# Kernel optimization log

Hardware: AMD Instinct MI355X
Metric: run time of the kernel (lower is better)

Reference implementation:

```python
import jax, jax.numpy as jnp
import numpy as np

B, N, D, KD = 8, 2048, 64, 64

def setup_inputs() -> dict:
    key = jax.random.key(0)
    ks = jax.random.split(key, 7)
    s = 1.0 / np.sqrt(D)
    return {
        "x":  jax.random.normal(ks[0], (B, N, D), dtype=jnp.float32),
        "Wq": jax.random.normal(ks[1], (D, KD), dtype=jnp.float32) * s,
        "bq": jnp.zeros((KD,), jnp.float32),
        "Wk": jax.random.normal(ks[2], (D, KD), dtype=jnp.float32) * s,
        "bk": jnp.zeros((KD,), jnp.float32),
        "Wv": jax.random.normal(ks[3], (D, KD), dtype=jnp.float32) * s,
        "bv": jnp.zeros((KD,), jnp.float32),
    }

def reference(x, Wq, bq, Wk, bk, Wv, bv):
    # Q,K,V: [B,N,KD]
    Q = x @ Wq + bq
    K = x @ Wk + bk
    V = x @ Wv + bv
    # scores: [B,N,N] (note: original applies NO 1/sqrt(d) scaling)
    scores = jnp.einsum('bij,bkj->bik', Q, K)
    probs = jax.nn.softmax(scores, axis=-1)
    # mean-threshold sparsification: keep entries above the row mean
    mask = (probs > jnp.mean(probs, axis=-1, keepdims=True)).astype(probs.dtype)
    sparse = probs * mask
    out = jnp.einsum('bij,bjk->bik', sparse, V)  # [B,N,KD]
    return out
```

## Files before the change

kernel.cpp:

```cpp
#include <hip/hip_runtime.h>

#define NB 8
#define NS 2048
#define ND 64
#define LOG2E 1.44269504f
#define QSC 256.0f
#define IQS (1.0f / 256.0f)

typedef _Float16 half8 __attribute__((ext_vector_type(8)));
typedef short short8 __attribute__((ext_vector_type(8)));
typedef __attribute__((ext_vector_type(4))) float floatx4;

__device__ __forceinline__ half8 cvt8(const float* p) {
    float4 a = *(const float4*)p;
    float4 b = *(const float4*)(p + 4);
    half8 h = {(_Float16)a.x, (_Float16)a.y, (_Float16)a.z, (_Float16)a.w,
               (_Float16)b.x, (_Float16)b.y, (_Float16)b.z, (_Float16)b.w};
    return h;
}
__device__ __forceinline__ half8 cvtWcol(const float* base) {
    half8 h;
#pragma unroll
    for (int j = 0; j < 8; ++j) h[j] = (_Float16)base[j * 64];
    return h;
}

__global__ __launch_bounds__(256) void qkv_proj(
    const float* __restrict__ x,
    const float* __restrict__ Wq, const float* __restrict__ bq,
    const float* __restrict__ Wk, const float* __restrict__ bk,
    const float* __restrict__ Wv, const float* __restrict__ bv,
    _Float16* __restrict__ Qg, _Float16* __restrict__ Kg,
    _Float16* __restrict__ Vt)
{
    __shared__ _Float16 vt[64 * 18];

    const int tid  = threadIdx.x;
    const int wv   = tid >> 6;
    const int l    = tid & 63;
    const int quad = l >> 4;
    const int tx   = l & 15;

    const int b  = blockIdx.x & 7;
    const int n0 = (blockIdx.x >> 3) * 16;

    const float* xr = x + ((size_t)b * NS + n0 + tx) * ND + quad * 8;
    half8 a0 = cvt8(xr);
    half8 a1 = cvt8(xr + 32);

    const floatx4 zf = {0.f, 0.f, 0.f, 0.f};

#pragma unroll
    for (int i = 0; i < 3; ++i) {
        const int ct = wv * 3 + i;
        const int m  = ct >> 2;
        const int lcol = (ct & 3) * 16 + tx;

        const float* Wm;
        const float* Bm;
        if (m == 0)      { Wm = Wq; Bm = bq; }
        else if (m == 1) { Wm = Wk; Bm = bk; }
        else             { Wm = Wv; Bm = bv; }

        half8 b0 = cvtWcol(Wm + (quad * 8) * 64 + lcol);
        half8 b1 = cvtWcol(Wm + (32 + quad * 8) * 64 + lcol);

        floatx4 acc = __builtin_amdgcn_mfma_f32_16x16x32_f16(a0, b0, zf, 0, 0, 0);
        acc = __builtin_amdgcn_mfma_f32_16x16x32_f16(a1, b1, acc, 0, 0, 0);
        const float bias = Bm[lcol];

        if (m == 0) {
#pragma unroll
            for (int r = 0; r < 4; ++r)
                Qg[((size_t)b * NS + n0 + quad * 4 + r) * ND + lcol] =
                    (_Float16)((acc[r] + bias) * LOG2E);
        } else if (m == 1) {
#pragma unroll
            for (int r = 0; r < 4; ++r)
                Kg[((size_t)b * NS + n0 + quad * 4 + r) * ND + lcol] = (_Float16)(acc[r] + bias);
        } else {
#pragma unroll
            for (int r = 0; r < 4; ++r)
                vt[lcol * 18 + quad * 4 + r] = (_Float16)(acc[r] + bias);
        }
    }
    __syncthreads();
    {
        const int d = tid >> 2, seg = tid & 3;
        uint2 p = *(uint2*)&vt[d * 18 + seg * 4];
        *(uint2*)(Vt + ((size_t)b * ND + d) * NS + n0 + seg * 4) = p;
    }
}

__global__ __launch_bounds__(512, 2) void attn(
    const _Float16* __restrict__ Qg,
    const _Float16* __restrict__ Kg,
    const _Float16* __restrict__ Vt,
    short* __restrict__ ct,
    float* __restrict__ out)
{
    __shared__ __align__(16) _Float16 smem[2 * 64 * 136];
    __shared__ float lsh[4 * 64];

    const int tid  = threadIdx.x;
    const int wv   = tid >> 6;
    const int l    = tid & 63;
    const int quad = l >> 4;
    const int tx   = l & 15;
    const int h    = wv >> 2;
    const int kq   = wv & 3;

    const int b  = blockIdx.x & 7;
    const int q0 = (blockIdx.x >> 3) * 64;

    const _Float16* Qb = Qg + ((size_t)b * NS + q0 + h * 32) * ND;
    const _Float16* Kb = Kg + (size_t)b * NS * ND;
    const _Float16* Vb = Vt + (size_t)b * ND * NS;
    short* ctb = ct + ((size_t)b * NS + q0) * NS;

    half8 qf[2][2];
#pragma unroll
    for (int rh = 0; rh < 2; ++rh)
#pragma unroll
        for (int kc = 0; kc < 2; ++kc)
            qf[rh][kc] = *(const half8*)(Qb + (size_t)(rh * 16 + tx) * ND + kc * 32 + quad * 8);

    const floatx4 zf = {0.f, 0.f, 0.f, 0.f};

    {
        const int skey = tid >> 3;
        const int sc   = (tid & 7) * 8;
        const _Float16* Ksrc = Kb + (size_t)skey * ND + sc;
        const int sdst = skey * 72 + sc;
        const int krow = (kq * 16 + tx) * 72;

        short* cst0 = ctb + (size_t)(h * 32 + tx) * NS + kq * 16 + quad * 4;
        short* cst1 = cst0 + (size_t)16 * NS;

        float lacc0 = 0.f, lacc1 = 0.f;

        uint4 gk = *(const uint4*)Ksrc;
        *(uint4*)(smem + sdst) = gk;
        for (int t = 0; t < 32; ++t) {
            const int buf = (t & 1) * 4608;
            __syncthreads();
            if (t < 31) gk = *(const uint4*)(Ksrc + (size_t)(t + 1) * 64 * ND);
            half8 kf0 = *(const half8*)(smem + buf + krow + quad * 8);
            half8 kf1 = *(const half8*)(smem + buf + krow + 32 + quad * 8);
#pragma unroll
            for (int rh = 0; rh < 2; ++rh) {
                floatx4 c = __builtin_amdgcn_mfma_f32_16x16x32_f16(kf0, qf[rh][0], zf, 0, 0, 0);
                c = __builtin_amdgcn_mfma_f32_16x16x32_f16(kf1, qf[rh][1], c, 0, 0, 0);
                int ci[4];
                float ladd = 0.f;
#pragma unroll
                for (int r = 0; r < 4; ++r) {
                    float cs = fminf(fmaxf(c[r] * QSC, -32767.f), 32767.f);
                    int ic = (int)rintf(cs);
                    ci[r] = ic;
                    ladd += __builtin_amdgcn_exp2f((float)ic * IQS);
                }
                if (rh == 0) lacc0 += ladd; else lacc1 += ladd;
                uint2 pk;
                pk.x = (unsigned)(ci[0] & 0xffff) | ((unsigned)(ci[1] & 0xffff) << 16);
                pk.y = (unsigned)(ci[2] & 0xffff) | ((unsigned)(ci[3] & 0xffff) << 16);
                *(uint2*)((rh ? cst1 : cst0) + (size_t)t * 64) = pk;
            }
            if (t < 31) *(uint4*)(smem + (buf ^ 4608) + sdst) = gk;
        }

#pragma unroll
        for (int off = 16; off < 64; off <<= 1) {
            lacc0 += __shfl_xor(lacc0, off);
            lacc1 += __shfl_xor(lacc1, off);
        }
        if (quad == 0) {
            lsh[kq * 64 + h * 32 + tx]      = lacc0;
            lsh[kq * 64 + h * 32 + 16 + tx] = lacc1;
        }
    }

    const int sdim = tid >> 4;
    const int sseg = (tid & 15) * 8;
    const _Float16* Vsrc0 = Vb + (size_t)sdim * NS + sseg;
    const _Float16* Vsrc1 = Vb + (size_t)(sdim + 32) * NS + sseg;
    const int vdst0 = sdim * 136 + sseg;
    const int vdst1 = (sdim + 32) * 136 + sseg;

    const short* crd0 = ctb + (size_t)(h * 32 + tx) * NS + kq * 32 + quad * 8;
    const short* crd1 = crd0 + (size_t)16 * NS;

    uint4 gv0 = *(const uint4*)Vsrc0;
    uint4 gv1 = *(const uint4*)Vsrc1;
    short8 ca0 = *(const short8*)crd0;
    short8 ca1 = *(const short8*)crd1;

    __syncthreads();

    float lg2L0, lg2L1;
    {
        const int row = h * 32 + tx;
        float L0 = lsh[row] + lsh[64 + row] + lsh[128 + row] + lsh[192 + row];
        float L1 = lsh[row + 16] + lsh[64 + row + 16] + lsh[128 + row + 16] + lsh[192 + row + 16];
        lg2L0 = __builtin_amdgcn_logf(L0);
        lg2L1 = __builtin_amdgcn_logf(L1);
    }

    *(uint4*)(smem + vdst0) = gv0;
    *(uint4*)(smem + vdst1) = gv1;

    floatx4 o[2][4] = {{zf, zf, zf, zf}, {zf, zf, zf, zf}};

    for (int t = 0; t < 16; ++t) {
        const int buf = (t & 1) * 8704;
        __syncthreads();
        short8 cn0, cn1;
        if (t < 15) {
            gv0 = *(const uint4*)(Vsrc0 + (size_t)(t + 1) * 128);
            gv1 = *(const uint4*)(Vsrc1 + (size_t)(t + 1) * 128);
            cn0 = *(const short8*)(crd0 + (size_t)(t + 1) * 128);
            cn1 = *(const short8*)(crd1 + (size_t)(t + 1) * 128);
        }
        half8 a0, a1;
#pragma unroll
        for (int j = 0; j < 8; ++j) {
            float d0 = (float)ca0[j] * IQS - lg2L0;
            a0[j] = (d0 > -11.f) ? (_Float16)__builtin_amdgcn_exp2f(d0) : (_Float16)0.f;
            float d1 = (float)ca1[j] * IQS - lg2L1;
            a1[j] = (d1 > -11.f) ? (_Float16)__builtin_amdgcn_exp2f(d1) : (_Float16)0.f;
        }
#pragma unroll
        for (int dg = 0; dg < 4; ++dg) {
            half8 vf = *(const half8*)(smem + buf + (dg * 16 + tx) * 136 + kq * 32 + quad * 8);
            o[0][dg] = __builtin_amdgcn_mfma_f32_16x16x32_f16(a0, vf, o[0][dg], 0, 0, 0);
            o[1][dg] = __builtin_amdgcn_mfma_f32_16x16x32_f16(a1, vf, o[1][dg], 0, 0, 0);
        }
        if (t < 15) {
            *(uint4*)(smem + (buf ^ 8704) + vdst0) = gv0;
            *(uint4*)(smem + (buf ^ 8704) + vdst1) = gv1;
            ca0 = cn0; ca1 = cn1;
        }
    }

    __syncthreads();
    float* osm = (float*)smem;
    if (kq == 0) {
#pragma unroll
        for (int rt = 0; rt < 2; ++rt)
#pragma unroll
            for (int dg = 0; dg < 4; ++dg)
#pragma unroll
                for (int r = 0; r < 4; ++r)
                    osm[(h * 32 + rt * 16 + quad * 4 + r) * 68 + dg * 16 + tx] = o[rt][dg][r];
    }
    __syncthreads();
    if (kq == 1) {
#pragma unroll
        for (int rt = 0; rt < 2; ++rt)
#pragma unroll
            for (int dg = 0; dg < 4; ++dg)
#pragma unroll
                for (int r = 0; r < 4; ++r)
                    osm[(h * 32 + rt * 16 + quad * 4 + r) * 68 + dg * 16 + tx] += o[rt][dg][r];
    }
    __syncthreads();
    if (kq == 2) {
#pragma unroll
        for (int rt = 0; rt < 2; ++rt)
#pragma unroll
            for (int dg = 0; dg < 4; ++dg)
#pragma unroll
                for (int r = 0; r < 4; ++r)
                    osm[(h * 32 + rt * 16 + quad * 4 + r) * 68 + dg * 16 + tx] += o[rt][dg][r];
    }
    __syncthreads();
    if (kq == 3) {
#pragma unroll
        for (int rt = 0; rt < 2; ++rt)
#pragma unroll
            for (int dg = 0; dg < 4; ++dg)
#pragma unroll
                for (int r = 0; r < 4; ++r)
                    out[((size_t)b * NS + q0 + h * 32 + rt * 16 + quad * 4 + r) * ND + dg * 16 + tx] =
                        osm[(h * 32 + rt * 16 + quad * 4 + r) * 68 + dg * 16 + tx] + o[rt][dg][r];
    }
}

extern "C" void kernel_launch(void* const* d_in, const int* in_sizes, int n_in,
                              void* d_out, int out_size, void* d_ws, size_t ws_size,
                              hipStream_t stream) {
    const float* x  = (const float*)d_in[0];
    const float* Wq = (const float*)d_in[1];
    const float* bq = (const float*)d_in[2];
    const float* Wk = (const float*)d_in[3];
    const float* bk = (const float*)d_in[4];
    const float* Wv = (const float*)d_in[5];
    const float* bv = (const float*)d_in[6];

    _Float16* Qg = (_Float16*)d_ws;
    _Float16* Kg = Qg + (size_t)NB * NS * ND;
    _Float16* Vt = Kg + (size_t)NB * NS * ND;
    short*    ct = (short*)(Vt + (size_t)NB * NS * ND);

    qkv_proj<<<NB * (NS / 16), 256, 0, stream>>>(x, Wq, bq, Wk, bk, Wv, bv, Qg, Kg, Vt);
    attn<<<NB * (NS / 64), 512, 0, stream>>>(Qg, Kg, Vt, ct, (float*)d_out);
}
```

Measured before the change: 122.8 us.

## Recompute QK^T scores in second pass instead of storing quantized scores

The attention kernel no longer writes int16-quantized scores to a global scratch buffer and rereads them. The second pass recomputes QK^T from K tiles in shared memory, applies exp2 with a mean threshold (L/N) and normalises by 1/L, then multiplies by V. This removes a large global write/read of B*N*N shorts at the cost of doubling the score MFMA work. A separate wprep kernel pre-transposes the weights to fp16, and qkv_proj now handles 64 rows per block to cut weight reloads.

```diff
diff --git a/kernel.cpp b/kernel.cpp
--- a/kernel.cpp
+++ b/kernel.cpp
@@ -4,11 +4,9 @@
 #define NS 2048
 #define ND 64
 #define LOG2E 1.44269504f
-#define QSC 256.0f
-#define IQS (1.0f / 256.0f)
 
 typedef _Float16 half8 __attribute__((ext_vector_type(8)));
-typedef short short8 __attribute__((ext_vector_type(8)));
+typedef _Float16 half4 __attribute__((ext_vector_type(4)));
 typedef __attribute__((ext_vector_type(4))) float floatx4;
 
 __device__ __forceinline__ half8 cvt8(const float* p) {
@@ -18,22 +16,27 @@
                (_Float16)b.x, (_Float16)b.y, (_Float16)b.z, (_Float16)b.w};
     return h;
 }
-__device__ __forceinline__ half8 cvtWcol(const float* base) {
-    half8 h;
-#pragma unroll
-    for (int j = 0; j < 8; ++j) h[j] = (_Float16)base[j * 64];
-    return h;
+
+__global__ __launch_bounds__(256) void wprep(
+    const float* __restrict__ Wq, const float* __restrict__ Wk,
+    const float* __restrict__ Wv, _Float16* __restrict__ Wt)
+{
+    const int m = blockIdx.x;
+    const float* W = (m == 0) ? Wq : (m == 1) ? Wk : Wv;
+    for (int i = threadIdx.x; i < 64 * 64; i += 256) {
+        const int c = i >> 6, d = i & 63;
+        Wt[((size_t)m * 64 + c) * 64 + d] = (_Float16)W[d * 64 + c];
+    }
 }
 
 __global__ __launch_bounds__(256) void qkv_proj(
-    const float* __restrict__ x,
-    const float* __restrict__ Wq, const float* __restrict__ bq,
-    const float* __restrict__ Wk, const float* __restrict__ bk,
-    const float* __restrict__ Wv, const float* __restrict__ bv,
+    const float* __restrict__ x, const _Float16* __restrict__ Wt,
+    const float* __restrict__ bq, const float* __restrict__ bk,
+    const float* __restrict__ bv,
     _Float16* __restrict__ Qg, _Float16* __restrict__ Kg,
     _Float16* __restrict__ Vt)
 {
-    __shared__ _Float16 vt[64 * 18];
+    __shared__ _Float16 vt[4][64 * 20];
 
     const int tid  = threadIdx.x;
     const int wv   = tid >> 6;
@@ -42,7 +45,7 @@
     const int tx   = l & 15;
 
     const int b  = blockIdx.x & 7;
-    const int n0 = (blockIdx.x >> 3) * 16;
+    const int n0 = (blockIdx.x >> 3) * 64 + wv * 16;
 
     const float* xr = x + ((size_t)b * NS + n0 + tx) * ND + quad * 8;
     half8 a0 = cvt8(xr);
@@ -51,23 +54,19 @@
     const floatx4 zf = {0.f, 0.f, 0.f, 0.f};
 
 #pragma unroll
-    for (int i = 0; i < 3; ++i) {
-        const int ct = wv * 3 + i;
-        const int m  = ct >> 2;
-        const int lcol = (ct & 3) * 16 + tx;
-
-        const float* Wm;
-        const float* Bm;
-        if (m == 0)      { Wm = Wq; Bm = bq; }
-        else if (m == 1) { Wm = Wk; Bm = bk; }
-        else             { Wm = Wv; Bm = bv; }
-
-        half8 b0 = cvtWcol(Wm + (quad * 8) * 64 + lcol);
-        half8 b1 = cvtWcol(Wm + (32 + quad * 8) * 64 + lcol);
+    for (int ctile = 0; ctile < 12; ++ctile) {
+        const int m    = ctile >> 2;
+        const int lcol = (ctile & 3) * 16 + tx;
+
+        const _Float16* Wb = Wt + ((size_t)m * 64 + lcol) * 64;
+        half8 b0 = *(const half8*)(Wb + quad * 8);
+        half8 b1 = *(const half8*)(Wb + 32 + quad * 8);
 
         floatx4 acc = __builtin_amdgcn_mfma_f32_16x16x32_f16(a0, b0, zf, 0, 0, 0);
         acc = __builtin_amdgcn_mfma_f32_16x16x32_f16(a1, b1, acc, 0, 0, 0);
-        const float bias = Bm[lcol];
+
+        const float* Bp = (m == 0) ? bq : (m == 1) ? bk : bv;
+        const float bias = Bp[lcol];
 
         if (m == 0) {
 #pragma unroll
@@ -77,18 +76,27 @@
         } else if (m == 1) {
 #pragma unroll
             for (int r = 0; r < 4; ++r)
-                Kg[((size_t)b * NS + n0 + quad * 4 + r) * ND + lcol] = (_Float16)(acc[r] + bias);
+                Kg[((size_t)b * NS + n0 + quad * 4 + r) * ND + lcol] =
+                    (_Float16)(acc[r] + bias);
         } else {
 #pragma unroll
             for (int r = 0; r < 4; ++r)
-                vt[lcol * 18 + quad * 4 + r] = (_Float16)(acc[r] + bias);
+                vt[wv][lcol * 20 + quad * 4 + r] = (_Float16)(acc[r] + bias);
         }
     }
     __syncthreads();
     {
-        const int d = tid >> 2, seg = tid & 3;
-        uint2 p = *(uint2*)&vt[d * 18 + seg * 4];
-        *(uint2*)(Vt + ((size_t)b * ND + d) * NS + n0 + seg * 4) = p;
+        const int d = l;
+        const _Float16* src = &vt[wv][d * 20];
+        uint2 p0 = *(const uint2*)(src);
+        uint2 p1 = *(const uint2*)(src + 4);
+        uint2 p2 = *(const uint2*)(src + 8);
+        uint2 p3 = *(const uint2*)(src + 12);
+        uint4 q0 = {p0.x, p0.y, p1.x, p1.y};
+        uint4 q1 = {p2.x, p2.y, p3.x, p3.y};
+        _Float16* dst = Vt + ((size_t)b * ND + d) * NS + n0;
+        *(uint4*)(dst)     = q0;
+        *(uint4*)(dst + 8) = q1;
     }
 }
 
@@ -96,11 +104,13 @@
     const _Float16* __restrict__ Qg,
     const _Float16* __restrict__ Kg,
     const _Float16* __restrict__ Vt,
-    short* __restrict__ ct,
     float* __restrict__ out)
 {
-    __shared__ __align__(16) _Float16 smem[2 * 64 * 136];
+    __shared__ __align__(16) _Float16 smem[2 * 64 * 72 + 2 * 64 * 72];
     __shared__ float lsh[4 * 64];
+
+    _Float16* ksm = smem;
+    _Float16* vsm = smem + 2 * 64 * 72;
 
     const int tid  = threadIdx.x;
     const int wv   = tid >> 6;
@@ -116,7 +126,6 @@
     const _Float16* Qb = Qg + ((size_t)b * NS + q0 + h * 32) * ND;
     const _Float16* Kb = Kg + (size_t)b * NS * ND;
     const _Float16* Vb = Vt + (size_t)b * ND * NS;
-    short* ctb = ct + ((size_t)b * NS + q0) * NS;
 
     half8 qf[2][2];
 #pragma unroll
@@ -125,120 +134,99 @@
         for (int kc = 0; kc < 2; ++kc)
             qf[rh][kc] = *(const half8*)(Qb + (size_t)(rh * 16 + tx) * ND + kc * 32 + quad * 8);
 
+    const int skey = tid >> 3;
+    const int sc   = (tid & 7) * 8;
+    const _Float16* Ksrc = Kb + (size_t)skey * ND + sc;
+    const _Float16* Vsrc = Vb + (size_t)skey * NS + sc;
+    const int kdst = skey * 72 + sc;
+
     const floatx4 zf = {0.f, 0.f, 0.f, 0.f};
-
+    const int krow = (kq * 16 + tx) * 72;
+
+    float lacc0 = 0.f, lacc1 = 0.f;
     {
-        const int skey = tid >> 3;
-        const int sc   = (tid & 7) * 8;
-        const _Float16* Ksrc = Kb + (size_t)skey * ND + sc;
-        const int sdst = skey * 72 + sc;
-        const int krow = (kq * 16 + tx) * 72;
-
-        short* cst0 = ctb + (size_t)(h * 32 + tx) * NS + kq * 16 + quad * 4;
-        short* cst1 = cst0 + (size_t)16 * NS;
-
-        float lacc0 = 0.f, lacc1 = 0.f;
-
         uint4 gk = *(const uint4*)Ksrc;
-        *(uint4*)(smem + sdst) = gk;
+        *(uint4*)(ksm + kdst) = gk;
         for (int t = 0; t < 32; ++t) {
             const int buf = (t & 1) * 4608;
             __syncthreads();
             if (t < 31) gk = *(const uint4*)(Ksrc + (size_t)(t + 1) * 64 * ND);
-            half8 kf0 = *(const half8*)(smem + buf + krow + quad * 8);
-            half8 kf1 = *(const half8*)(smem + buf + krow + 32 + quad * 8);
+            half8 kf0 = *(const half8*)(ksm + buf + krow + quad * 8);
+            half8 kf1 = *(const half8*)(ksm + buf + krow + 32 + quad * 8);
 #pragma unroll
             for (int rh = 0; rh < 2; ++rh) {
                 floatx4 c = __builtin_amdgcn_mfma_f32_16x16x32_f16(kf0, qf[rh][0], zf, 0, 0, 0);
                 c = __builtin_amdgcn_mfma_f32_16x16x32_f16(kf1, qf[rh][1], c, 0, 0, 0);
-                int ci[4];
-                float ladd = 0.f;
-#pragma unroll
-                for (int r = 0; r < 4; ++r) {
-                    float cs = fminf(fmaxf(c[r] * QSC, -32767.f), 32767.f);
-                    int ic = (int)rintf(cs);
-                    ci[r] = ic;
-                    ladd += __builtin_amdgcn_exp2f((float)ic * IQS);
-                }
+                float ladd = __builtin_amdgcn_exp2f(c[0]) + __builtin_amdgcn_exp2f(c[1])
+                           + __builtin_amdgcn_exp2f(c[2]) + __builtin_amdgcn_exp2f(c[3]);
                 if (rh == 0) lacc0 += ladd; else lacc1 += ladd;
-                uint2 pk;
-                pk.x = (unsigned)(ci[0] & 0xffff) | ((unsigned)(ci[1] & 0xffff) << 16);
-                pk.y = (unsigned)(ci[2] & 0xffff) | ((unsigned)(ci[3] & 0xffff) << 16);
-                *(uint2*)((rh ? cst1 : cst0) + (size_t)t * 64) = pk;
             }
-            if (t < 31) *(uint4*)(smem + (buf ^ 4608) + sdst) = gk;
-        }
-
-#pragma unroll
-        for (int off = 16; off < 64; off <<= 1) {
-            lacc0 += __shfl_xor(lacc0, off);
-            lacc1 += __shfl_xor(lacc1, off);
-        }
-        if (quad == 0) {
-            lsh[kq * 64 + h * 32 + tx]      = lacc0;
-            lsh[kq * 64 + h * 32 + 16 + tx] = lacc1;
-        }
-    }
-
-    const int sdim = tid >> 4;
-    const int sseg = (tid & 15) * 8;
-    const _Float16* Vsrc0 = Vb + (size_t)sdim * NS + sseg;
-    const _Float16* Vsrc1 = Vb + (size_t)(sdim + 32) * NS + sseg;
-    const int vdst0 = sdim * 136 + sseg;
-    const int vdst1 = (sdim + 32) * 136 + sseg;
-
-    const short* crd0 = ctb + (size_t)(h * 32 + tx) * NS + kq * 32 + quad * 8;
-    const short* crd1 = crd0 + (size_t)16 * NS;
-
-    uint4 gv0 = *(const uint4*)Vsrc0;
-    uint4 gv1 = *(const uint4*)Vsrc1;
-    short8 ca0 = *(const short8*)crd0;
-    short8 ca1 = *(const short8*)crd1;
-
-    __syncthreads();
-
-    float lg2L0, lg2L1;
+            if (t < 31) *(uint4*)(ksm + (buf ^ 4608) + kdst) = gk;
+        }
+    }
+#pragma unroll
+    for (int off = 16; off < 64; off <<= 1) {
+        lacc0 += __shfl_xor(lacc0, off);
+        lacc1 += __shfl_xor(lacc1, off);
+    }
+    if (quad == 0) {
+        lsh[kq * 64 + h * 32 + tx]      = lacc0;
+        lsh[kq * 64 + h * 32 + 16 + tx] = lacc1;
+    }
+
+    uint4 gk = *(const uint4*)Ksrc;
+    uint4 gv = *(const uint4*)Vsrc;
+    __syncthreads();
+
+    float thr0, inv0, thr1, inv1;
     {
         const int row = h * 32 + tx;
         float L0 = lsh[row] + lsh[64 + row] + lsh[128 + row] + lsh[192 + row];
         float L1 = lsh[row + 16] + lsh[64 + row + 16] + lsh[128 + row + 16] + lsh[192 + row + 16];
-        lg2L0 = __builtin_amdgcn_logf(L0);
-        lg2L1 = __builtin_amdgcn_logf(L1);
-    }
-
-    *(uint4*)(smem + vdst0) = gv0;
-    *(uint4*)(smem + vdst1) = gv1;
+        inv0 = 1.f / L0;  thr0 = L0 * (1.f / (float)NS);
+        inv1 = 1.f / L1;  thr1 = L1 * (1.f / (float)NS);
+    }
+
+    *(uint4*)(ksm + kdst) = gk;
+    *(uint4*)(vsm + kdst) = gv;
 
     floatx4 o[2][4] = {{zf, zf, zf, zf}, {zf, zf, zf, zf}};
 
-    for (int t = 0; t < 16; ++t) {
-        const int buf = (t & 1) * 8704;
+    for (int t = 0; t < 32; ++t) {
+        const int buf = (t & 1) * 4608;
         __syncthreads();
-        short8 cn0, cn1;
-        if (t < 15) {
-            gv0 = *(const uint4*)(Vsrc0 + (size_t)(t + 1) * 128);
-            gv1 = *(const uint4*)(Vsrc1 + (size_t)(t + 1) * 128);
-            cn0 = *(const short8*)(crd0 + (size_t)(t + 1) * 128);
-            cn1 = *(const short8*)(crd1 + (size_t)(t + 1) * 128);
-        }
-        half8 a0, a1;
-#pragma unroll
-        for (int j = 0; j < 8; ++j) {
-            float d0 = (float)ca0[j] * IQS - lg2L0;
-            a0[j] = (d0 > -11.f) ? (_Float16)__builtin_amdgcn_exp2f(d0) : (_Float16)0.f;
-            float d1 = (float)ca1[j] * IQS - lg2L1;
-            a1[j] = (d1 > -11.f) ? (_Float16)__builtin_amdgcn_exp2f(d1) : (_Float16)0.f;
-        }
-#pragma unroll
-        for (int dg = 0; dg < 4; ++dg) {
-            half8 vf = *(const half8*)(smem + buf + (dg * 16 + tx) * 136 + kq * 32 + quad * 8);
-            o[0][dg] = __builtin_amdgcn_mfma_f32_16x16x32_f16(a0, vf, o[0][dg], 0, 0, 0);
-            o[1][dg] = __builtin_amdgcn_mfma_f32_16x16x32_f16(a1, vf, o[1][dg], 0, 0, 0);
-        }
-        if (t < 15) {
-            *(uint4*)(smem + (buf ^ 8704) + vdst0) = gv0;
-            *(uint4*)(smem + (buf ^ 8704) + vdst1) = gv1;
-            ca0 = cn0; ca1 = cn1;
+        if (t < 31) {
+            gk = *(const uint4*)(Ksrc + (size_t)(t + 1) * 64 * ND);
+            gv = *(const uint4*)(Vsrc + (size_t)(t + 1) * 64);
+        }
+        half8 kf0 = *(const half8*)(ksm + buf + krow + quad * 8);
+        half8 kf1 = *(const half8*)(ksm + buf + krow + 32 + quad * 8);
+        half4 vf[4];
+#pragma unroll
+        for (int dg = 0; dg < 4; ++dg)
+            vf[dg] = *(const half4*)(vsm + buf + (dg * 16 + tx) * 72 + kq * 16 + quad * 4);
+#pragma unroll
+        for (int rh = 0; rh < 2; ++rh) {
+            floatx4 c = __builtin_amdgcn_mfma_f32_16x16x32_f16(kf0, qf[rh][0], zf, 0, 0, 0);
+            c = __builtin_amdgcn_mfma_f32_16x16x32_f16(kf1, qf[rh][1], c, 0, 0, 0);
+            const float thr = rh ? thr1 : thr0;
+            const float inv = rh ? inv1 : inv0;
+            float e0 = __builtin_amdgcn_exp2f(c[0]);
+            float e1 = __builtin_amdgcn_exp2f(c[1]);
+            float e2 = __builtin_amdgcn_exp2f(c[2]);
+            float e3 = __builtin_amdgcn_exp2f(c[3]);
+            float w0 = (e0 > thr) ? e0 * inv : 0.f;
+            float w1 = (e1 > thr) ? e1 * inv : 0.f;
+            float w2 = (e2 > thr) ? e2 * inv : 0.f;
+            float w3 = (e3 > thr) ? e3 * inv : 0.f;
+            half4 af = {(_Float16)w0, (_Float16)w1, (_Float16)w2, (_Float16)w3};
+#pragma unroll
+            for (int dg = 0; dg < 4; ++dg)
+                o[rh][dg] = __builtin_amdgcn_mfma_f32_16x16x16f16(af, vf[dg], o[rh][dg], 0, 0, 0);
+        }
+        if (t < 31) {
+            *(uint4*)(ksm + (buf ^ 4608) + kdst) = gk;
+            *(uint4*)(vsm + (buf ^ 4608) + kdst) = gv;
         }
     }
 
@@ -246,43 +234,43 @@
     float* osm = (float*)smem;
     if (kq == 0) {
 #pragma unroll
-        for (int rt = 0; rt < 2; ++rt)
-#pragma unroll
-            for (int dg = 0; dg < 4; ++dg)
-#pragma unroll
-                for (int r = 0; r < 4; ++r)
-                    osm[(h * 32 + rt * 16 + quad * 4 + r) * 68 + dg * 16 + tx] = o[rt][dg][r];
+        for (int rh = 0; rh < 2; ++rh)
+#pragma unroll
+            for (int dg = 0; dg < 4; ++dg)
+#pragma unroll
+                for (int r = 0; r < 4; ++r)
+                    osm[(h * 32 + rh * 16 + quad * 4 + r) * 68 + dg * 16 + tx] = o[rh][dg][r];
     }
     __syncthreads();
     if (kq == 1) {
 #pragma unroll
-        for (int rt = 0; rt < 2; ++rt)
-#pragma unroll
-            for (int dg = 0; dg < 4; ++dg)
-#pragma unroll
-                for (int r = 0; r < 4; ++r)
-                    osm[(h * 32 + rt * 16 + quad * 4 + r) * 68 + dg * 16 + tx] += o[rt][dg][r];
+        for (int rh = 0; rh < 2; ++rh)
+#pragma unroll
+            for (int dg = 0; dg < 4; ++dg)
+#pragma unroll
+                for (int r = 0; r < 4; ++r)
+                    osm[(h * 32 + rh * 16 + quad * 4 + r) * 68 + dg * 16 + tx] += o[rh][dg][r];
     }
     __syncthreads();
     if (kq == 2) {
 #pragma unroll
-        for (int rt = 0; rt < 2; ++rt)
-#pragma unroll
-            for (int dg = 0; dg < 4; ++dg)
-#pragma unroll
-                for (int r = 0; r < 4; ++r)
-                    osm[(h * 32 + rt * 16 + quad * 4 + r) * 68 + dg * 16 + tx] += o[rt][dg][r];
+        for (int rh = 0; rh < 2; ++rh)
+#pragma unroll
+            for (int dg = 0; dg < 4; ++dg)
+#pragma unroll
+                for (int r = 0; r < 4; ++r)
+                    osm[(h * 32 + rh * 16 + quad * 4 + r) * 68 + dg * 16 + tx] += o[rh][dg][r];
     }
     __syncthreads();
     if (kq == 3) {
 #pragma unroll
-        for (int rt = 0; rt < 2; ++rt)
-#pragma unroll
-            for (int dg = 0; dg < 4; ++dg)
-#pragma unroll
-                for (int r = 0; r < 4; ++r)
-                    out[((size_t)b * NS + q0 + h * 32 + rt * 16 + quad * 4 + r) * ND + dg * 16 + tx] =
-                        osm[(h * 32 + rt * 16 + quad * 4 + r) * 68 + dg * 16 + tx] + o[rt][dg][r];
+        for (int rh = 0; rh < 2; ++rh)
+#pragma unroll
+            for (int dg = 0; dg < 4; ++dg)
+#pragma unroll
+                for (int r = 0; r < 4; ++r)
+                    out[((size_t)b * NS + q0 + h * 32 + rh * 16 + quad * 4 + r) * ND + dg * 16 + tx] =
+                        osm[(h * 32 + rh * 16 + quad * 4 + r) * 68 + dg * 16 + tx] + o[rh][dg][r];
     }
 }
 
@@ -300,8 +288,9 @@
     _Float16* Qg = (_Float16*)d_ws;
     _Float16* Kg = Qg + (size_t)NB * NS * ND;
     _Float16* Vt = Kg + (size_t)NB * NS * ND;
-    short*    ct = (short*)(Vt + (size_t)NB * NS * ND);
-
-    qkv_proj<<<NB * (NS / 16), 256, 0, stream>>>(x, Wq, bq, Wk, bk, Wv, bv, Qg, Kg, Vt);
-    attn<<<NB * (NS / 64), 512, 0, stream>>>(Qg, Kg, Vt, ct, (float*)d_out);
-}
+    _Float16* Wt = Vt + (size_t)NB * NS * ND;
+
+    wprep<<<3, 256, 0, stream>>>(Wq, Wk, Wv, Wt);
+    qkv_proj<<<NB * (NS / 64), 256, 0, stream>>>(x, Wt, bq, bk, bv, Qg, Kg, Vt);
+    attn<<<NB * (NS / 64), 512, 0, stream>>>(Qg, Kg, Vt, (float*)d_out);
+}
```

Result: faster. 112.4 us (-8.5%).
